# Kernel optimization log

Hardware: AMD Instinct MI355X
Metric: run time of the kernel (lower is better)

The kernel has to match this reference:

```python
import jax, jax.numpy as jnp
import numpy as np

B, S, DIM, H = 1, 4096, 1024, 16
HEAD_DIM = DIM // H
ROPE_THETA = 10000.0
LN_EPS = 1e-5


def _rope_cos_sin(seq_len, dim, theta):
    # frequencies over the FULL model dim (rope applied before head split, as in source)
    inv_freq = 1.0 / (theta ** (jnp.arange(0, dim, 2, dtype=jnp.float32) / dim))  # (dim/2,)
    ang = jnp.arange(seq_len, dtype=jnp.float32)[:, None] * inv_freq[None, :]     # (S, dim/2)
    cos = jnp.concatenate([jnp.cos(ang), jnp.cos(ang)], axis=-1)                  # (S, dim)
    sin = jnp.concatenate([jnp.sin(ang), jnp.sin(ang)], axis=-1)
    return cos, sin


def _rotate_half(x):
    d = x.shape[-1] // 2
    return jnp.concatenate([-x[..., d:], x[..., :d]], axis=-1)


def _apply_rope(x, cos, sin):
    # x: (B, S, dim); cos/sin: (S, dim)
    return x * cos[None] + _rotate_half(x) * sin[None]


def setup_inputs() -> dict:
    key = jax.random.key(0)
    ks = jax.random.split(key, 5)
    sc = 1.0 / np.sqrt(DIM)
    return {
        "x": jax.random.normal(ks[0], (B, S, DIM), dtype=jnp.float32),
        "Wqkv": jax.random.normal(ks[1], (DIM, 3 * DIM), dtype=jnp.float32) * sc,
        "bqkv": jax.random.normal(ks[2], (3 * DIM,), dtype=jnp.float32) * 0.01,
        "Wo": jax.random.normal(ks[3], (DIM, DIM), dtype=jnp.float32) * sc,
        "bo": jax.random.normal(ks[4], (DIM,), dtype=jnp.float32) * 0.01,
        "gamma": jnp.ones((DIM,), dtype=jnp.float32),
        "beta": jnp.zeros((DIM,), dtype=jnp.float32),
    }


def reference(x, Wqkv, bqkv, Wo, bo, gamma, beta):
    b, s, d = x.shape
    qkv = x @ Wqkv + bqkv                      # (B, S, 3*dim)
    q, k, v = jnp.split(qkv, 3, axis=-1)       # each (B, S, dim)
    cos, sin = _rope_cos_sin(s, d, ROPE_THETA)
    q = _apply_rope(q, cos, sin)
    k = _apply_rope(k, cos, sin)
    # split heads
    q = q.reshape(b, s, H, HEAD_DIM)
    k = k.reshape(b, s, H, HEAD_DIM)
    v = v.reshape(b, s, H, HEAD_DIM)
    scale = 1.0 / np.sqrt(HEAD_DIM)
    scores = jnp.einsum('bqhd,bkhd->bhqk', q, k) * scale  # (B, H, S, S)
    causal = jnp.triu(jnp.ones((s, s), dtype=bool), k=1)
    scores = jnp.where(causal[None, None], -jnp.inf, scores)
    attn = jax.nn.softmax(scores, axis=-1)
    out = jnp.einsum('bhqk,bkhd->bqhd', attn, v).reshape(b, s, d)
    out = out @ Wo + bo
    # LayerNorm (dropout is identity in eval mode)
    mu = jnp.mean(out, axis=-1, keepdims=True)
    var = jnp.mean(jnp.square(out - mu), axis=-1, keepdims=True)
    return (out - mu) * jax.lax.rsqrt(var + LN_EPS) * gamma + beta
```

## Files before the change

### kernel.cpp

```cpp
#include <hip/hip_runtime.h>
#include <cstdint>
#include <cstddef>

#define S_LEN 4096
#define DIM   1024
#define NH    16
#define HD    64
#define QKV_N 3072
#define NSPLIT 4

typedef __attribute__((ext_vector_type(8))) short short8;
typedef __attribute__((ext_vector_type(4))) float f32x4;
typedef __attribute__((ext_vector_type(4))) unsigned short ushort4v;
typedef __attribute__((ext_vector_type(2))) unsigned int uint2v;
typedef __attribute__((ext_vector_type(4))) _Float16 half4;
typedef __attribute__((ext_vector_type(2))) _Float16 half2v;

__device__ inline unsigned short f2bf(float x) {
    unsigned int u = __builtin_bit_cast(unsigned int, x);
    u += 0x7fffu + ((u >> 16) & 1u);
    return (unsigned short)(u >> 16);
}
__device__ inline float bf2f(unsigned short u) {
    return __builtin_bit_cast(float, (unsigned int)u << 16);
}
__device__ inline unsigned int pack2_bf16_rh(float lo, float hi) {
    unsigned int a = __builtin_bit_cast(unsigned int, lo) + 0x8000u;
    unsigned int b = __builtin_bit_cast(unsigned int, hi) + 0x8000u;
    return __builtin_amdgcn_perm(b, a, 0x07060302u);
}

__device__ inline void gl_lds16(const void* g, void* l) {
    __builtin_amdgcn_global_load_lds(
        (const __attribute__((address_space(1))) void*)g,
        (__attribute__((address_space(3))) void*)l, 16, 0, 0);
}

template <bool BF16OUT>
__global__ __launch_bounds__(256) void gemm_mfma_kernel(
    const unsigned short* __restrict__ A,
    const unsigned short* __restrict__ Bt,
    const float* __restrict__ bias,
    void* __restrict__ Cv,
    int M, int N, int K)
{
    __shared__ unsigned short As[128 * 32];
    __shared__ unsigned short Bs[128 * 32];

    const int t    = threadIdx.x;
    const int w    = t >> 6;
    const int lane = t & 63;
    const int ln   = lane & 15;
    const int quad = lane >> 4;
    const int bm   = blockIdx.y * 128;
    const int bn   = blockIdx.x * 128;
    const int wm   = (w & 1) * 64;
    const int wn   = (w >> 1) * 64;

    f32x4 acc[4][4];
#pragma unroll
    for (int i = 0; i < 4; ++i)
#pragma unroll
        for (int j = 0; j < 4; ++j) acc[i][j] = (f32x4){0.f, 0.f, 0.f, 0.f};

    const int lr = lane >> 2;
    const int lc = (lane & 3) * 8;
    const unsigned short* ga = A  + (size_t)(bm + w * 32 + lr) * K + lc;
    const unsigned short* gb = Bt + (size_t)(bn + w * 32 + lr) * K + lc;
    unsigned short* la = &As[(w * 32) * 32];
    unsigned short* lb = &Bs[(w * 32) * 32];

    for (int k0 = 0; k0 < K; k0 += 32) {
        gl_lds16(ga,            la);
        gl_lds16(ga + 16 * K,   la + 16 * 32);
        gl_lds16(gb,            lb);
        gl_lds16(gb + 16 * K,   lb + 16 * 32);
        ga += 32; gb += 32;
        __syncthreads();

        short8 af[4], bf[4];
#pragma unroll
        for (int i = 0; i < 4; ++i)
            af[i] = *(const short8*)&As[(wm + i * 16 + ln) * 32 + quad * 8];
#pragma unroll
        for (int j = 0; j < 4; ++j)
            bf[j] = *(const short8*)&Bs[(wn + j * 16 + ln) * 32 + quad * 8];
#pragma unroll
        for (int i = 0; i < 4; ++i)
#pragma unroll
            for (int j = 0; j < 4; ++j)
                acc[i][j] = __builtin_amdgcn_mfma_f32_16x16x32_bf16(af[i], bf[j], acc[i][j], 0, 0, 0);
        __syncthreads();
    }

#pragma unroll
    for (int j = 0; j < 4; ++j) {
        const int col = bn + wn + j * 16 + ln;
        const float bv = bias[col];
#pragma unroll
        for (int i = 0; i < 4; ++i) {
            const int row0 = bm + wm + i * 16 + quad * 4;
#pragma unroll
            for (int r = 0; r < 4; ++r) {
                const float v = acc[i][j][r] + bv;
                if (BF16OUT)
                    ((unsigned short*)Cv)[(size_t)(row0 + r) * N + col] = f2bf(v);
                else
                    ((float*)Cv)[(size_t)(row0 + r) * N + col] = v;
            }
        }
    }
}

__global__ __launch_bounds__(256) void prep1_kernel(
    const float* __restrict__ x, unsigned short* __restrict__ xb,
    const float* __restrict__ Wqkv, unsigned short* __restrict__ WqkvT,
    const float* __restrict__ Wo, unsigned short* __restrict__ WoT)
{
    __shared__ unsigned short L[64][72];
    const int b = blockIdx.x;
    const int t = threadIdx.x;

    if (b < 2048) {
        const size_t i = ((size_t)b * 256 + t) * 8;
        float4 a = *(const float4*)(x + i);
        float4 c = *(const float4*)(x + i + 4);
        short8 p = { (short)f2bf(a.x), (short)f2bf(a.y), (short)f2bf(a.z), (short)f2bf(a.w),
                     (short)f2bf(c.x), (short)f2bf(c.y), (short)f2bf(c.z), (short)f2bf(c.w) };
        *(short8*)(xb + i) = p;
        return;
    }
    const float* W;
    unsigned short* Wt;
    int N, n0, k0;
    if (b < 2816) {
        const int wb = b - 2048;
        W = Wqkv; Wt = WqkvT; N = QKV_N;
        n0 = (wb % 48) * 64; k0 = (wb / 48) * 64;
    } else {
        const int wb = b - 2816;
        W = Wo; Wt = WoT; N = DIM;
        n0 = (wb & 15) * 64; k0 = (wb >> 4) * 64;
    }
    const int kr = t >> 2, cb = (t & 3) * 16;
    const float* wp = W + (size_t)(k0 + kr) * N + n0 + cb;
#pragma unroll
    for (int u = 0; u < 16; u += 4) {
        float4 v = *(const float4*)(wp + u);
        ushort4v p = { f2bf(v.x), f2bf(v.y), f2bf(v.z), f2bf(v.w) };
        *(ushort4v*)&L[kr][cb + u] = p;
    }
    __syncthreads();
    const int nr = t >> 2, kb = (t & 3) * 16;
    short8 lo, hi;
#pragma unroll
    for (int u = 0; u < 8; ++u) lo[u] = (short)L[kb + u][nr];
#pragma unroll
    for (int u = 0; u < 8; ++u) hi[u] = (short)L[kb + 8 + u][nr];
    unsigned short* op = Wt + (size_t)(n0 + nr) * 1024 + k0 + kb;
    *(short8*)op       = lo;
    *(short8*)(op + 8) = hi;
}

__global__ __launch_bounds__(256) void prep2_kernel(
    const unsigned short* __restrict__ qkvb,
    unsigned short* __restrict__ Qb,
    unsigned short* __restrict__ Kb,
    unsigned short* __restrict__ Vt)
{
    __shared__ unsigned short L[64][72];
    const int b = blockIdx.x;
    const int t = threadIdx.x;

    if (b < 2048) {
        const int idx = b * 256 + t;
        const int j   = (idx & 127) * 4;
        const int s   = idx >> 7;
        const unsigned short* row = qkvb + (size_t)s * QKV_N;
        unsigned short* qo = Qb + (size_t)s * DIM;
        unsigned short* ko = Kb + (size_t)s * DIM;
        const float sf = (float)s;
        const float QSCALE = 0.18033688011112042f;
        const float C1 = -0.025952563241307517f;
        const float INV2PI = 0.15915494309189535f;

        float cs[4], sn[4];
#pragma unroll
        for (int e = 0; e < 4; ++e) {
            const float invf2pi = exp2f((float)(j + e) * C1) * INV2PI;
            float rev = sf * invf2pi;
            rev -= floorf(rev);
            sn[e] = __builtin_amdgcn_sinf(rev);
            cs[e] = __builtin_amdgcn_cosf(rev);
        }
        ushort4v q1 = *(const ushort4v*)(row + j);
        ushort4v q2 = *(const ushort4v*)(row + 512 + j);
        ushort4v k1 = *(const ushort4v*)(row + DIM + j);
        ushort4v k2 = *(const ushort4v*)(row + DIM + 512 + j);
        ushort4v qa, qb4, ka, kb4;
#pragma unroll
        for (int e = 0; e < 4; ++e) {
            const float x1 = bf2f(q1[e]), x2 = bf2f(q2[e]);
            const float y1 = bf2f(k1[e]), y2 = bf2f(k2[e]);
            qa[e]  = f2bf((x1 * cs[e] - x2 * sn[e]) * QSCALE);
            qb4[e] = f2bf((x2 * cs[e] + x1 * sn[e]) * QSCALE);
            ka[e]  = f2bf(y1 * cs[e] - y2 * sn[e]);
            kb4[e] = f2bf(y2 * cs[e] + y1 * sn[e]);
        }
        *(ushort4v*)(qo + j)       = qa;
        *(ushort4v*)(qo + 512 + j) = qb4;
        *(ushort4v*)(ko + j)       = ka;
        *(ushort4v*)(ko + 512 + j) = kb4;
        return;
    }

    const int vb = b - 2048;
    const int c0 = (vb & 15) * 64;
    const int bs = (vb >> 4) * 64;
    const int sl = t >> 2, cb = (t & 3) * 16;
    const unsigned short* vp = qkvb + (size_t)(bs + sl) * QKV_N + 2 * DIM + c0 + cb;
    *(short8*)&L[sl][cb]     = *(const short8*)vp;
    *(short8*)&L[sl][cb + 8] = *(const short8*)(vp + 8);
    __syncthreads();
    const int cl = t >> 2, sb = (t & 3) * 16;
    short8 lo, hi;
#pragma unroll
    for (int u = 0; u < 8; ++u)
        lo[u] = (short)__builtin_bit_cast(unsigned short, (_Float16)bf2f(L[sb + u][cl]));
#pragma unroll
    for (int u = 0; u < 8; ++u)
        hi[u] = (short)__builtin_bit_cast(unsigned short, (_Float16)bf2f(L[sb + 8 + u][cl]));
    unsigned short* op = Vt + (size_t)(c0 + cl) * S_LEN + bs + sb;
    *(short8*)op       = lo;
    *(short8*)(op + 8) = hi;
}

__global__ __launch_bounds__(256) void attn_mfma_kernel(
    const unsigned short* __restrict__ Qb,
    const unsigned short* __restrict__ Kb,
    const unsigned short* __restrict__ Vt,
    unsigned short* __restrict__ Opb,
    float* __restrict__ lp)
{
    __shared__ unsigned short Ks[64][72];
    __shared__ unsigned short Vs[64][72];

    const int t    = threadIdx.x;
    const int w    = t >> 6;
    const int lane = t & 63;
    const int ln   = lane & 15;
    const int quad = lane >> 4;
    const int p    = blockIdx.x;
    const int hf   = blockIdx.y;
    const int h    = blockIdx.z;

    const int srow = t >> 2;
    const int scol = (t & 3) * 16;

    for (int phase = 0; phase < 2; ++phase) {
        const int qt  = phase == 0 ? (63 - p) : p;
        const int q0  = qt * 64;
        const int nkt = qt + 1;
        const int kt_begin = (nkt * hf) >> 2;
        const int kt_end   = (nkt * (hf + 1)) >> 2;

        short8 qf[2];
        {
            const unsigned short* qp = Qb + (size_t)(q0 + w * 16 + ln) * DIM + h * HD + quad * 8;
            qf[0] = *(const short8*)qp;
            qf[1] = *(const short8*)(qp + 32);
        }

        f32x4 o[4];
#pragma unroll
        for (int db = 0; db < 4; ++db) o[db] = (f32x4){0.f, 0.f, 0.f, 0.f};
        float lac = 0.f;

        short8 kr0, kr1, vr0, vr1;
        {
            const int k0 = kt_begin * 64;
            const unsigned short* kp = Kb + (size_t)(k0 + srow) * DIM + h * HD + scol;
            kr0 = *(const short8*)kp;       kr1 = *(const short8*)(kp + 8);
            const unsigned short* vp = Vt + (size_t)(h * HD + srow) * S_LEN + k0 + scol;
            vr0 = *(const short8*)vp;       vr1 = *(const short8*)(vp + 8);
        }

        for (int kt = kt_begin; kt < kt_end; ++kt) {
            __syncthreads();
            *(short8*)&Ks[srow][scol]     = kr0;
            *(short8*)&Ks[srow][scol + 8] = kr1;
            *(short8*)&Vs[srow][scol]     = vr0;
            *(short8*)&Vs[srow][scol + 8] = vr1;
            if (kt + 1 < kt_end) {
                const int k1 = (kt + 1) * 64;
                const unsigned short* kp = Kb + (size_t)(k1 + srow) * DIM + h * HD + scol;
                kr0 = *(const short8*)kp;   kr1 = *(const short8*)(kp + 8);
                const unsigned short* vp = Vt + (size_t)(h * HD + srow) * S_LEN + k1 + scol;
                vr0 = *(const short8*)vp;   vr1 = *(const short8*)(vp + 8);
            }
            __syncthreads();

            f32x4 sc[4];
#pragma unroll
            for (int kb = 0; kb < 4; ++kb) sc[kb] = (f32x4){0.f, 0.f, 0.f, 0.f};
#pragma unroll
            for (int kk = 0; kk < 2; ++kk) {
#pragma unroll
                for (int kb = 0; kb < 4; ++kb) {
                    short8 kf = *(const short8*)&Ks[kb * 16 + ln][kk * 32 + quad * 8];
                    sc[kb] = __builtin_amdgcn_mfma_f32_16x16x32_bf16(kf, qf[kk], sc[kb], 0, 0, 0);
                }
            }

            if (kt == nkt - 1) {
                const int qg = q0 + w * 16 + ln;
#pragma unroll
                for (int kb = 0; kb < 4; ++kb) {
                    const int key = kt * 64 + kb * 16 + quad * 4;
#pragma unroll
                    for (int r = 0; r < 4; ++r)
                        if (key + r > qg) sc[kb][r] = -1e30f;
                }
            }

            half4 pf[4];
#pragma unroll
            for (int kb = 0; kb < 4; ++kb) {
                const float p0 = exp2f(sc[kb][0]);
                const float p1 = exp2f(sc[kb][1]);
                const float p2 = exp2f(sc[kb][2]);
                const float p3 = exp2f(sc[kb][3]);
                lac += (p0 + p1) + (p2 + p3);
                half2v lo2 = __builtin_bit_cast(half2v, __builtin_amdgcn_cvt_pkrtz(p0, p1));
                half2v hi2 = __builtin_bit_cast(half2v, __builtin_amdgcn_cvt_pkrtz(p2, p3));
                pf[kb] = (half4){lo2[0], lo2[1], hi2[0], hi2[1]};
            }

#pragma unroll
            for (int db = 0; db < 4; ++db) {
#pragma unroll
                for (int kb = 0; kb < 4; ++kb) {
                    half4 vf = *(const half4*)&Vs[db * 16 + ln][kb * 16 + quad * 4];
                    o[db] = __builtin_amdgcn_mfma_f32_16x16x16f16(vf, pf[kb], o[db], 0, 0, 0);
                }
            }
        }

        lac += __shfl_xor(lac, 16);
        lac += __shfl_xor(lac, 32);

        unsigned short* op = Opb + ((size_t)hf * S_LEN + q0 + w * 16 + ln) * DIM
                                 + h * HD + quad * 4;
#pragma unroll
        for (int db = 0; db < 4; ++db) {
            uint2v pk = { pack2_bf16_rh(o[db][0], o[db][1]),
                          pack2_bf16_rh(o[db][2], o[db][3]) };
            *(uint2v*)(op + db * 16) = pk;
        }
        if (quad == 0)
            lp[((size_t)hf * NH + h) * S_LEN + q0 + w * 16 + ln] = lac;
    }
}

__global__ __launch_bounds__(256) void combine_kernel(
    const unsigned short* __restrict__ Opb, const float* __restrict__ lp,
    unsigned short* __restrict__ attnb)
{
    const int row = blockIdx.x;
    const int t   = threadIdx.x;
    const int d   = t * 4;
    const int h   = t >> 4;
    f32x4 acc = (f32x4){0.f, 0.f, 0.f, 0.f};
    float l = 0.f;
#pragma unroll
    for (int i = 0; i < NSPLIT; ++i) {
        ushort4v a = *(const ushort4v*)&Opb[((size_t)i * S_LEN + row) * DIM + d];
#pragma unroll
        for (int e = 0; e < 4; ++e) acc[e] += bf2f(a[e]);
        l += lp[((size_t)i * NH + h) * S_LEN + row];
    }
    const float inv = 1.0f / l;
    ushort4v o;
#pragma unroll
    for (int e = 0; e < 4; ++e) o[e] = f2bf(acc[e] * inv);
    *(ushort4v*)&attnb[(size_t)row * DIM + d] = o;
}

__global__ __launch_bounds__(256) void ln_kernel(
    const float* __restrict__ in, const float* __restrict__ gamma,
    const float* __restrict__ beta, float* __restrict__ out)
{
    const int row = blockIdx.x;
    const int t = threadIdx.x;
    const float4 v = *(const float4*)&in[(size_t)row * DIM + t * 4];
    float s  = v.x + v.y + v.z + v.w;
    float sq = v.x * v.x + v.y * v.y + v.z * v.z + v.w * v.w;
#pragma unroll
    for (int off = 1; off < 64; off <<= 1) {
        s  += __shfl_xor(s, off);
        sq += __shfl_xor(sq, off);
    }
    __shared__ float red[8];
    const int wv = t >> 6, ln = t & 63;
    if (ln == 0) { red[wv] = s; red[4 + wv] = sq; }
    __syncthreads();
    s  = red[0] + red[1] + red[2] + red[3];
    sq = red[4] + red[5] + red[6] + red[7];
    const float mu  = s * (1.0f / DIM);
    const float var = sq * (1.0f / DIM) - mu * mu;
    const float rs  = rsqrtf(var + 1e-5f);
    const float4 g = *(const float4*)&gamma[t * 4];
    const float4 b = *(const float4*)&beta[t * 4];
    float4 o = { (v.x - mu) * rs * g.x + b.x,
                 (v.y - mu) * rs * g.y + b.y,
                 (v.z - mu) * rs * g.z + b.z,
                 (v.w - mu) * rs * g.w + b.w };
    *(float4*)&out[(size_t)row * DIM + t * 4] = o;
}

extern "C" void kernel_launch(void* const* d_in, const int* in_sizes, int n_in,
                              void* d_out, int out_size, void* d_ws, size_t ws_size,
                              hipStream_t stream)
{
    const float* x     = (const float*)d_in[0];
    const float* Wqkv  = (const float*)d_in[1];
    const float* bqkv  = (const float*)d_in[2];
    const float* Wo    = (const float*)d_in[3];
    const float* bo    = (const float*)d_in[4];
    const float* gamma = (const float*)d_in[5];
    const float* beta  = (const float*)d_in[6];
    float* out = (float*)d_out;

    char* base = (char*)d_ws;
    unsigned short* qkvb  = (unsigned short*)base;
    unsigned short* attnb = (unsigned short*)base;
    unsigned short* Opb   = (unsigned short*)(base + (size_t)8 * 1024 * 1024);
    float* proj = (float*)(base + (size_t)8 * 1024 * 1024);
    float* lp   = (float*)(base + (size_t)40 * 1024 * 1024);
    unsigned short* Qb    = (unsigned short*)(base + (size_t)48 * 1024 * 1024);
    unsigned short* Kb    = (unsigned short*)(base + (size_t)56 * 1024 * 1024);
    unsigned short* Vt    = (unsigned short*)(base + (size_t)64 * 1024 * 1024);
    unsigned short* xb    = (unsigned short*)(base + (size_t)72 * 1024 * 1024);
    unsigned short* WqkvT = (unsigned short*)(base + (size_t)80 * 1024 * 1024);
    unsigned short* WoT   = (unsigned short*)(base + (size_t)86 * 1024 * 1024);

    prep1_kernel<<<3072, 256, 0, stream>>>(x, xb, Wqkv, WqkvT, Wo, WoT);

    gemm_mfma_kernel<true><<<dim3(QKV_N / 128, S_LEN / 128), 256, 0, stream>>>(
        xb, WqkvT, bqkv, qkvb, S_LEN, QKV_N, DIM);

    prep2_kernel<<<3072, 256, 0, stream>>>(qkvb, Qb, Kb, Vt);

    attn_mfma_kernel<<<dim3(32, NSPLIT, NH), 256, 0, stream>>>(Qb, Kb, Vt, Opb, lp);

    combine_kernel<<<S_LEN, 256, 0, stream>>>(Opb, lp, attnb);

    gemm_mfma_kernel<false><<<dim3(DIM / 128, S_LEN / 128), 256, 0, stream>>>(
        attnb, WoT, bo, proj, S_LEN, DIM, DIM);

    ln_kernel<<<S_LEN, 256, 0, stream>>>(proj, gamma, beta, out);
}
```

Measured before the change: 257.7 us.

## Process 128 query rows per attention block to reuse K/V tiles across two sub-tiles

The attention kernel now gives each block two 64-row query sub-tiles (128 rows), so every K/V tile loaded into shared memory feeds twice as many MFMAs. V fragments are hoisted into registers once per tile, and the score, mask, exp and PV steps are interleaved per key block. The grid is halved to 16 blocks along x, which lowers parallelism and raises register pressure. The causal masking now checks the last two key tiles.

```diff
diff --git a/kernel.cpp b/kernel.cpp
--- a/kernel.cpp
+++ b/kernel.cpp
@@ -258,23 +258,27 @@
     const int scol = (t & 3) * 16;
 
     for (int phase = 0; phase < 2; ++phase) {
-        const int qt  = phase == 0 ? (63 - p) : p;
-        const int q0  = qt * 64;
-        const int nkt = qt + 1;
+        const int qt  = phase == 0 ? (31 - p) : p;
+        const int q0  = qt * 128;
+        const int nkt = 2 * (qt + 1);
         const int kt_begin = (nkt * hf) >> 2;
         const int kt_end   = (nkt * (hf + 1)) >> 2;
 
-        short8 qf[2];
-        {
-            const unsigned short* qp = Qb + (size_t)(q0 + w * 16 + ln) * DIM + h * HD + quad * 8;
-            qf[0] = *(const short8*)qp;
-            qf[1] = *(const short8*)(qp + 32);
-        }
-
-        f32x4 o[4];
-#pragma unroll
-        for (int db = 0; db < 4; ++db) o[db] = (f32x4){0.f, 0.f, 0.f, 0.f};
-        float lac = 0.f;
+        short8 qf[2][2];
+#pragma unroll
+        for (int s = 0; s < 2; ++s) {
+            const unsigned short* qp = Qb + (size_t)(q0 + s * 64 + w * 16 + ln) * DIM
+                                          + h * HD + quad * 8;
+            qf[s][0] = *(const short8*)qp;
+            qf[s][1] = *(const short8*)(qp + 32);
+        }
+
+        f32x4 o[2][4];
+#pragma unroll
+        for (int s = 0; s < 2; ++s)
+#pragma unroll
+            for (int db = 0; db < 4; ++db) o[s][db] = (f32x4){0.f, 0.f, 0.f, 0.f};
+        float lac[2] = {0.f, 0.f};
 
         short8 kr0, kr1, vr0, vr1;
         {
@@ -300,65 +304,63 @@
             }
             __syncthreads();
 
-            f32x4 sc[4];
-#pragma unroll
-            for (int kb = 0; kb < 4; ++kb) sc[kb] = (f32x4){0.f, 0.f, 0.f, 0.f};
-#pragma unroll
-            for (int kk = 0; kk < 2; ++kk) {
+            half4 vf[4][4];
+#pragma unroll
+            for (int db = 0; db < 4; ++db)
+#pragma unroll
+                for (int kb = 0; kb < 4; ++kb)
+                    vf[db][kb] = *(const half4*)&Vs[db * 16 + ln][kb * 16 + quad * 4];
+
+            const bool need_mask = (kt >= nkt - 2);
+
+#pragma unroll
+            for (int s = 0; s < 2; ++s) {
+                const int qg = q0 + s * 64 + w * 16 + ln;
 #pragma unroll
                 for (int kb = 0; kb < 4; ++kb) {
-                    short8 kf = *(const short8*)&Ks[kb * 16 + ln][kk * 32 + quad * 8];
-                    sc[kb] = __builtin_amdgcn_mfma_f32_16x16x32_bf16(kf, qf[kk], sc[kb], 0, 0, 0);
+                    f32x4 sc = (f32x4){0.f, 0.f, 0.f, 0.f};
+#pragma unroll
+                    for (int kk = 0; kk < 2; ++kk) {
+                        short8 kf = *(const short8*)&Ks[kb * 16 + ln][kk * 32 + quad * 8];
+                        sc = __builtin_amdgcn_mfma_f32_16x16x32_bf16(kf, qf[s][kk], sc, 0, 0, 0);
+                    }
+                    if (need_mask) {
+                        const int key = kt * 64 + kb * 16 + quad * 4;
+#pragma unroll
+                        for (int r = 0; r < 4; ++r)
+                            if (key + r > qg) sc[r] = -1e30f;
+                    }
+                    const float p0 = exp2f(sc[0]);
+                    const float p1 = exp2f(sc[1]);
+                    const float p2 = exp2f(sc[2]);
+                    const float p3 = exp2f(sc[3]);
+                    lac[s] += (p0 + p1) + (p2 + p3);
+                    half2v lo2 = __builtin_bit_cast(half2v, __builtin_amdgcn_cvt_pkrtz(p0, p1));
+                    half2v hi2 = __builtin_bit_cast(half2v, __builtin_amdgcn_cvt_pkrtz(p2, p3));
+                    half4 pf = (half4){lo2[0], lo2[1], hi2[0], hi2[1]};
+#pragma unroll
+                    for (int db = 0; db < 4; ++db)
+                        o[s][db] = __builtin_amdgcn_mfma_f32_16x16x16f16(vf[db][kb], pf, o[s][db], 0, 0, 0);
                 }
             }
-
-            if (kt == nkt - 1) {
-                const int qg = q0 + w * 16 + ln;
-#pragma unroll
-                for (int kb = 0; kb < 4; ++kb) {
-                    const int key = kt * 64 + kb * 16 + quad * 4;
-#pragma unroll
-                    for (int r = 0; r < 4; ++r)
-                        if (key + r > qg) sc[kb][r] = -1e30f;
-                }
+        }
+
+#pragma unroll
+        for (int s = 0; s < 2; ++s) {
+            lac[s] += __shfl_xor(lac[s], 16);
+            lac[s] += __shfl_xor(lac[s], 32);
+
+            unsigned short* op = Opb + ((size_t)hf * S_LEN + q0 + s * 64 + w * 16 + ln) * DIM
+                                     + h * HD + quad * 4;
+#pragma unroll
+            for (int db = 0; db < 4; ++db) {
+                uint2v pk = { pack2_bf16_rh(o[s][db][0], o[s][db][1]),
+                              pack2_bf16_rh(o[s][db][2], o[s][db][3]) };
+                *(uint2v*)(op + db * 16) = pk;
             }
-
-            half4 pf[4];
-#pragma unroll
-            for (int kb = 0; kb < 4; ++kb) {
-                const float p0 = exp2f(sc[kb][0]);
-                const float p1 = exp2f(sc[kb][1]);
-                const float p2 = exp2f(sc[kb][2]);
-                const float p3 = exp2f(sc[kb][3]);
-                lac += (p0 + p1) + (p2 + p3);
-                half2v lo2 = __builtin_bit_cast(half2v, __builtin_amdgcn_cvt_pkrtz(p0, p1));
-                half2v hi2 = __builtin_bit_cast(half2v, __builtin_amdgcn_cvt_pkrtz(p2, p3));
-                pf[kb] = (half4){lo2[0], lo2[1], hi2[0], hi2[1]};
-            }
-
-#pragma unroll
-            for (int db = 0; db < 4; ++db) {
-#pragma unroll
-                for (int kb = 0; kb < 4; ++kb) {
-                    half4 vf = *(const half4*)&Vs[db * 16 + ln][kb * 16 + quad * 4];
-                    o[db] = __builtin_amdgcn_mfma_f32_16x16x16f16(vf, pf[kb], o[db], 0, 0, 0);
-                }
-            }
-        }
-
-        lac += __shfl_xor(lac, 16);
-        lac += __shfl_xor(lac, 32);
-
-        unsigned short* op = Opb + ((size_t)hf * S_LEN + q0 + w * 16 + ln) * DIM
-                                 + h * HD + quad * 4;
-#pragma unroll
-        for (int db = 0; db < 4; ++db) {
-            uint2v pk = { pack2_bf16_rh(o[db][0], o[db][1]),
-                          pack2_bf16_rh(o[db][2], o[db][3]) };
-            *(uint2v*)(op + db * 16) = pk;
-        }
-        if (quad == 0)
-            lp[((size_t)hf * NH + h) * S_LEN + q0 + w * 16 + ln] = lac;
+            if (quad == 0)
+                lp[((size_t)hf * NH + h) * S_LEN + q0 + s * 64 + w * 16 + ln] = lac[s];
+        }
     }
 }
 
@@ -451,7 +453,7 @@
 
     prep2_kernel<<<3072, 256, 0, stream>>>(qkvb, Qb, Kb, Vt);
 
-    attn_mfma_kernel<<<dim3(32, NSPLIT, NH), 256, 0, stream>>>(Qb, Kb, Vt, Opb, lp);
+    attn_mfma_kernel<<<dim3(16, NSPLIT, NH), 256, 0, stream>>>(Qb, Kb, Vt, Opb, lp);
 
     combine_kernel<<<S_LEN, 256, 0, stream>>>(Opb, lp, attnb);
 
```

Measured after the change: 258.1 us. About the same (+0.1%).
